# Kernel tuning notes

Hardware: AMD Instinct MI355X
Metric: run time of the kernel (lower is better)

Reference implementation:

```python
import jax, jax.numpy as jnp
import numpy as np

D_EMB = 1024
N_HEAD = 16
D_K = D_EMB // N_HEAD


def setup_inputs() -> dict:
    key = jax.random.key(0)
    ks = jax.random.split(key, 11)
    B, S = 2, 2048
    s = 1.0 / np.sqrt(D_EMB)
    inp = {
        'Q': jax.random.normal(ks[0], (B, S, D_EMB), jnp.float32),
        'K': jax.random.normal(ks[1], (B, S, D_EMB), jnp.float32),
        'V': jax.random.normal(ks[2], (B, S, D_EMB), jnp.float32),
        'W_Q': jax.random.normal(ks[3], (D_EMB, D_EMB), jnp.float32) * s,
        'b_Q': jax.random.normal(ks[4], (D_EMB,), jnp.float32) * s,
        'W_K': jax.random.normal(ks[5], (D_EMB, D_EMB), jnp.float32) * s,
        'b_K': jax.random.normal(ks[6], (D_EMB,), jnp.float32) * s,
        'W_V': jax.random.normal(ks[7], (D_EMB, D_EMB), jnp.float32) * s,
        'b_V': jax.random.normal(ks[8], (D_EMB,), jnp.float32) * s,
        'W_O': jax.random.normal(ks[9], (D_EMB, D_EMB), jnp.float32) * s,
        'b_O': jax.random.normal(ks[10], (D_EMB,), jnp.float32) * s,
    }
    return inp


def _heads(x):
    # [B, S, D] -> [B, H, S, d_k]
    B, S, _ = x.shape
    return x.reshape(B, S, N_HEAD, D_K).transpose(0, 2, 1, 3)


def reference(Q, K, V, W_Q, b_Q, W_K, b_K, W_V, b_V, W_O, b_O):
    q = _heads(Q @ W_Q.T + b_Q)
    k = _heads(K @ W_K.T + b_K)
    v = _heads(V @ W_V.T + b_V)
    scale = 1.0 / jnp.sqrt(jnp.asarray(D_K, q.dtype))
    scores = jnp.einsum('bhqd,bhkd->bhqk', q, k) * scale  # [B,H,S,S]
    probs = jax.nn.softmax(scores, axis=-1)
    attn = jnp.einsum('bhqk,bhkd->bhqd', probs, v)
    B, H, S, d = attn.shape
    attn = attn.transpose(0, 2, 1, 3).reshape(B, S, H * d)
    return attn @ W_O.T + b_O
```

## Files before the change

kernel.cpp:

```cpp
#include <hip/hip_runtime.h>
#include <cstdint>
#include <cstddef>

#define S_LEN 2048
#define NH    16
#define DKH   64
#define DEMB  1024
#define MTOT  4096

typedef float f32x4 __attribute__((ext_vector_type(4)));
typedef __bf16 bf16x8 __attribute__((ext_vector_type(8)));
typedef _Float16 f16;
typedef f16 f16x2 __attribute__((ext_vector_type(2)));
typedef f16 f16x4 __attribute__((ext_vector_type(4)));
typedef f16 f16x8 __attribute__((ext_vector_type(8)));
typedef unsigned short u16;
typedef unsigned int u32;
typedef u16 u16x8 __attribute__((ext_vector_type(8)));
typedef u16 u16x4 __attribute__((ext_vector_type(4)));
typedef u32 u32x4 __attribute__((ext_vector_type(4)));

static __device__ __forceinline__ u16 f2bf(float f) {
  u32 u = __builtin_bit_cast(u32, f);
  u += 0x7fffu + ((u >> 16) & 1u);
  return (u16)(u >> 16);
}
static __device__ __forceinline__ float bf2f(u16 b) {
  return __builtin_bit_cast(float, ((u32)b) << 16);
}
static __device__ __forceinline__ bf16x8 ldfrag(const u16* p) {
  return __builtin_bit_cast(bf16x8, *(const u16x8*)p);
}
static __device__ __forceinline__ f16x8 ldfragh8(const u16* p) {
  return __builtin_bit_cast(f16x8, *(const u16x8*)p);
}
static __device__ __forceinline__ f32x4 mfma16(bf16x8 a, bf16x8 b, f32x4 c) {
  return __builtin_amdgcn_mfma_f32_16x16x32_bf16(a, b, c, 0, 0, 0);
}
static __device__ __forceinline__ f32x4 mfmah32(f16x8 a, f16x8 b, f32x4 c) {
  return __builtin_amdgcn_mfma_f32_16x16x32_f16(a, b, c, 0, 0, 0);
}
static __device__ __forceinline__ void gl2lds16(const void* g, void* l) {
  __builtin_amdgcn_global_load_lds((__attribute__((address_space(1))) void*)g,
                                   (__attribute__((address_space(3))) void*)l,
                                   16, 0, 0);
}
static __device__ __forceinline__ u32 pkh2(float a, float b) {
  return __builtin_bit_cast(u32, __builtin_amdgcn_cvt_pkrtz(a, b));
}
static __device__ __forceinline__ f16x4 pkh4(float a, float b, float c, float d) {
  f16x2 lo = __builtin_bit_cast(f16x2, __builtin_amdgcn_cvt_pkrtz(a, b));
  f16x2 hi = __builtin_bit_cast(f16x2, __builtin_amdgcn_cvt_pkrtz(c, d));
  return __builtin_shufflevector(lo, hi, 0, 1, 2, 3);
}

#define SCL_Q (0.125f * 1.44269504088896340736f)

__global__ __launch_bounds__(256) void cvt_w(
    const float* __restrict__ wq, const float* __restrict__ wk,
    const float* __restrict__ wv, u16* __restrict__ dW) {
  const int b = blockIdx.x;
  const int seg = b >> 10;
  const float* s = (seg == 0) ? wq : (seg == 1) ? wk : wv;
  u16* d = dW + (size_t)seg * (DEMB * DEMB);
  const int i = ((b & 1023) * 256 + threadIdx.x) * 4;
  f32x4 f = *(const f32x4*)(s + i);
  u16x4 o;
  o[0] = f2bf(f[0]); o[1] = f2bf(f[1]); o[2] = f2bf(f[2]); o[3] = f2bf(f[3]);
  *(u16x4*)(d + i) = o;
}

__global__ __launch_bounds__(256) void qkv_gemm(
    const float* __restrict__ qf, const float* __restrict__ kf,
    const float* __restrict__ vf, const u16* __restrict__ W,
    const float* __restrict__ bq, const float* __restrict__ bk,
    const float* __restrict__ bv,
    u16* __restrict__ qh, u16* __restrict__ kh, u16* __restrict__ vt) {
  __shared__ __align__(16) u16 sA0[128 * 32], sA1[128 * 32];
  __shared__ __align__(16) u16 sB0[128 * 32], sB1[128 * 32];
  const int t = threadIdx.x;
  const int l = t & 63, w = t >> 6;
  const int ll = l & 15, lg = l >> 4;
  const int orig = blockIdx.x + 24 * blockIdx.y;
  const int xcd = orig & 7, q = orig >> 3;
  const int nb = q >> 2;
  const int mb = xcd * 4 + (q & 3);
  const int which = nb >> 3;
  const float* A = (which == 0) ? qf : ((which == 1) ? kf : vf);
  const int wr = (w >> 1) * 64, wc = (w & 1) * 64;

  f32x4 acc[4][4] = {};

  const int c0 = t, c1 = 256 + t;
  const int row0 = c0 >> 2, row1 = c1 >> 2;
  const int gc0 = (c0 & 3) ^ ((row0 >> 1) & 3);
  const int gc1 = (c1 & 3) ^ ((row1 >> 1) & 3);
  const float* asrc0 = A + (size_t)(mb * 128 + row0) * DEMB + gc0 * 8;
  const float* asrc1 = A + (size_t)(mb * 128 + row1) * DEMB + gc1 * 8;
  const u16* bsrc0 = W + (size_t)(nb * 128 + row0) * DEMB + gc0 * 8;
  const u16* bsrc1 = W + (size_t)(nb * 128 + row1) * DEMB + gc1 * 8;

  f32x4 va[4];
  auto LOADA = [&](int kt) {
    const int k0 = kt * 32;
    va[0] = *(const f32x4*)(asrc0 + k0);
    va[1] = *(const f32x4*)(asrc0 + k0 + 4);
    va[2] = *(const f32x4*)(asrc1 + k0);
    va[3] = *(const f32x4*)(asrc1 + k0 + 4);
  };
  auto STOREA = [&](u16* dA) {
#pragma unroll
    for (int i = 0; i < 2; ++i) {
      u16x8 o;
#pragma unroll
      for (int r = 0; r < 4; ++r) o[r] = f2bf(va[2 * i][r]);
#pragma unroll
      for (int r = 0; r < 4; ++r) o[4 + r] = f2bf(va[2 * i + 1][r]);
      *(u16x8*)&dA[(i * 256 + t) * 8] = o;
    }
  };
  auto STGB = [&](int kt, u16* dB) {
    const int k0 = kt * 32;
    gl2lds16(bsrc0 + k0, dB + c0 * 8);
    gl2lds16(bsrc1 + k0, dB + c1 * 8);
  };

  auto comp = [&](const u16* cA, const u16* cB) {
    bf16x8 af[4], bfr[4];
#pragma unroll
    for (int i2 = 0; i2 < 4; ++i2) {
      const int row = wr + i2 * 16 + ll;
      af[i2] = ldfrag(&cA[row * 32 + (lg ^ ((row >> 1) & 3)) * 8]);
    }
#pragma unroll
    for (int j2 = 0; j2 < 4; ++j2) {
      const int row = wc + j2 * 16 + ll;
      bfr[j2] = ldfrag(&cB[row * 32 + (lg ^ ((row >> 1) & 3)) * 8]);
    }
#pragma unroll
    for (int i2 = 0; i2 < 4; ++i2)
#pragma unroll
      for (int j2 = 0; j2 < 4; ++j2)
        acc[i2][j2] = mfma16(af[i2], bfr[j2], acc[i2][j2]);
  };

  LOADA(0); STGB(0, sB0); STOREA(sA0);
  __syncthreads();
  for (int kt2 = 0; kt2 < 16; ++kt2) {
    LOADA(2 * kt2 + 1);
    STGB(2 * kt2 + 1, sB1);
    comp(sA0, sB0);
    STOREA(sA1);
    __syncthreads();
    if (kt2 < 15) { LOADA(2 * kt2 + 2); STGB(2 * kt2 + 2, sB0); }
    comp(sA1, sB1);
    if (kt2 < 15) STOREA(sA0);
    __syncthreads();
  }

  const float* bias = (which == 0) ? bq : ((which == 1) ? bk : bv);
  const int b = (mb * 128) >> 11;

  if (which == 2) {
#pragma unroll
    for (int j2 = 0; j2 < 4; ++j2) {
      const int nl = (nb * 128 + wc + j2 * 16 + ll) & 1023;
      const int h = nl >> 6, dk = nl & 63;
      const float bb = bias[nl];
      u16* base = vt + ((size_t)((b * NH + h) * DKH + dk)) * S_LEN;
#pragma unroll
      for (int i2 = 0; i2 < 4; ++i2) {
        const int s = (mb * 128 + wr + i2 * 16 + lg * 4) & 2047;
        const f16x4 pk = pkh4(acc[i2][j2][0] + bb, acc[i2][j2][1] + bb,
                              acc[i2][j2][2] + bb, acc[i2][j2][3] + bb);
        *(u16x4*)&base[s] = __builtin_bit_cast(u16x4, pk);
      }
    }
  } else {
    u16* outp = (which == 0) ? qh : kh;
    const float scl = (which == 0) ? SCL_Q : 1.0f;
#pragma unroll
    for (int j2 = 0; j2 < 4; ++j2) {
      const int nl = (nb * 128 + wc + j2 * 16 + ll) & 1023;
      const int h = nl >> 6, dk = nl & 63;
      const float bb = bias[nl];
#pragma unroll
      for (int i2 = 0; i2 < 4; ++i2) {
#pragma unroll
        for (int r = 0; r < 4; ++r) {
          const int s = (mb * 128 + wr + i2 * 16 + lg * 4 + r) & 2047;
          const float val = (acc[i2][j2][r] + bb) * scl;
          outp[((size_t)((b * NH + h) * S_LEN + s)) * DKH + dk] = f2bf(val);
        }
      }
    }
  }
}

__global__ __launch_bounds__(512, 4) void attn_kernel(
    const u16* __restrict__ qh, const u16* __restrict__ kh,
    const u16* __restrict__ vt, u16* __restrict__ opart,
    float* __restrict__ lpart) {
  __shared__ __align__(16) u16 sK0[64 * 64], sK1[64 * 64];
  __shared__ __align__(16) u16 sV0[64 * 64], sV1[64 * 64];
  const int t = threadIdx.x;
  const int l = t & 63, w = t >> 6;
  const int ll = l & 15, lg = l >> 4;
  const int qb = blockIdx.x >> 1;
  const int ks = blockIdx.x & 1;
  const int q_blk = qb * 256;
  const int bh = blockIdx.y;

  bf16x8 aq[2][2];
#pragma unroll
  for (int qt = 0; qt < 2; ++qt) {
    const u16* qbase =
        qh + ((size_t)bh * S_LEN + q_blk + w * 32 + qt * 16 + ll) * DKH;
    aq[qt][0] = ldfrag(qbase + lg * 8);
    aq[qt][1] = ldfrag(qbase + 32 + lg * 8);
  }

  f32x4 oT[2][4] = {};
  float l_part[2] = {0.f, 0.f};

  const int strow = t >> 3;
  const int sgc = (t & 7) ^ (strow & 7);
  const u16* kstg =
      kh + ((size_t)bh * S_LEN + ks * 1024 + strow) * DKH + sgc * 8;
  const u16* vstg =
      vt + ((size_t)bh * DKH + strow) * S_LEN + ks * 1024 + sgc * 8;

  auto stg = [&](int kt, u16* dK, u16* dV) {
    gl2lds16(kstg + (size_t)kt * 64 * DKH, dK + t * 8);
    gl2lds16(vstg + kt * 64, dV + t * 8);
  };

  auto compute = [&](const u16* cK, const u16* cV) {
#pragma unroll
    for (int pr = 0; pr < 2; ++pr) {
      u32 pw0[4], pw1[4];
#pragma unroll
      for (int h = 0; h < 2; ++h) {
        const int krow = (pr * 2 + h) * 16 + ll;
        const bf16x8 ak0 = ldfrag(&cK[krow * 64 + (lg ^ (ll & 7)) * 8]);
        const bf16x8 ak1 = ldfrag(&cK[krow * 64 + ((4 + lg) ^ (ll & 7)) * 8]);
        f32x4 s0 = {}, s1 = {};
        s0 = mfma16(ak0, aq[0][0], s0);
        s0 = mfma16(ak1, aq[0][1], s0);
        s1 = mfma16(ak0, aq[1][0], s1);
        s1 = mfma16(ak1, aq[1][1], s1);
        {
          const float p0 = __builtin_amdgcn_exp2f(s0[0]);
          const float p1 = __builtin_amdgcn_exp2f(s0[1]);
          const float p2 = __builtin_amdgcn_exp2f(s0[2]);
          const float p3 = __builtin_amdgcn_exp2f(s0[3]);
          l_part[0] += (p0 + p1) + (p2 + p3);
          if (h == 0) { pw0[0] = pkh2(p0, p1); pw0[1] = pkh2(p2, p3); }
          else        { pw0[2] = pkh2(p0, p1); pw0[3] = pkh2(p2, p3); }
        }
        {
          const float p0 = __builtin_amdgcn_exp2f(s1[0]);
          const float p1 = __builtin_amdgcn_exp2f(s1[1]);
          const float p2 = __builtin_amdgcn_exp2f(s1[2]);
          const float p3 = __builtin_amdgcn_exp2f(s1[3]);
          l_part[1] += (p0 + p1) + (p2 + p3);
          if (h == 0) { pw1[0] = pkh2(p0, p1); pw1[1] = pkh2(p2, p3); }
          else        { pw1[2] = pkh2(p0, p1); pw1[3] = pkh2(p2, p3); }
        }
      }
      asm volatile("v_permlane32_swap_b32 %0, %1" : "+v"(pw0[0]), "+v"(pw0[2]));
      asm volatile("v_permlane16_swap_b32 %0, %1" : "+v"(pw0[0]), "+v"(pw0[2]));
      asm volatile("v_permlane32_swap_b32 %0, %1" : "+v"(pw0[1]), "+v"(pw0[3]));
      asm volatile("v_permlane16_swap_b32 %0, %1" : "+v"(pw0[1]), "+v"(pw0[3]));
      asm volatile("v_permlane32_swap_b32 %0, %1" : "+v"(pw1[0]), "+v"(pw1[2]));
      asm volatile("v_permlane16_swap_b32 %0, %1" : "+v"(pw1[0]), "+v"(pw1[2]));
      asm volatile("v_permlane32_swap_b32 %0, %1" : "+v"(pw1[1]), "+v"(pw1[3]));
      asm volatile("v_permlane16_swap_b32 %0, %1" : "+v"(pw1[1]), "+v"(pw1[3]));
      const f16x8 bp0 =
          __builtin_bit_cast(f16x8, (u32x4){pw0[0], pw0[1], pw0[2], pw0[3]});
      const f16x8 bp1 =
          __builtin_bit_cast(f16x8, (u32x4){pw1[0], pw1[1], pw1[2], pw1[3]});

#pragma unroll
      for (int nt = 0; nt < 4; ++nt) {
        const int row = nt * 16 + ll;
        const f16x8 av =
            ldfragh8(&cV[row * 64 + ((pr * 4 + lg) ^ (ll & 7)) * 8]);
        oT[0][nt] = mfmah32(av, bp0, oT[0][nt]);
        oT[1][nt] = mfmah32(av, bp1, oT[1][nt]);
      }
    }
  };

  stg(0, sK0, sV0);
  __syncthreads();
  for (int kt2 = 0; kt2 < 8; ++kt2) {
    stg(2 * kt2 + 1, sK1, sV1);
    compute(sK0, sV0);
    __syncthreads();
    if (kt2 < 7) stg(2 * kt2 + 2, sK0, sV0);
    compute(sK1, sV1);
    __syncthreads();
  }

#pragma unroll
  for (int qt = 0; qt < 2; ++qt) {
    float lv = l_part[qt];
    lv += __shfl_xor(lv, 16, 64);
    lv += __shfl_xor(lv, 32, 64);
    const int orow = q_blk + w * 32 + qt * 16 + ll;
    u16* obase = opart + (((size_t)(ks * 32 + bh)) * S_LEN + orow) * DKH;
#pragma unroll
    for (int nt = 0; nt < 4; ++nt) {
      u16x4 o;
#pragma unroll
      for (int r = 0; r < 4; ++r) o[r] = f2bf(oT[qt][nt][r]);
      *(u16x4*)&obase[nt * 16 + lg * 4] = o;
    }
    if (lg == 0) lpart[(ks * 32 + bh) * S_LEN + orow] = lv;
  }
}

__global__ __launch_bounds__(256) void merge_ctx(
    const u16* __restrict__ op, const float* __restrict__ lp,
    u16* __restrict__ ctx, const float* __restrict__ wo,
    u16* __restrict__ woBf) {
  if (blockIdx.x >= 2048) {
    const int i = ((blockIdx.x - 2048) * 256 + threadIdx.x) * 4;
    f32x4 f = *(const f32x4*)(wo + i);
    u16x4 o;
    o[0] = f2bf(f[0]); o[1] = f2bf(f[1]); o[2] = f2bf(f[2]); o[3] = f2bf(f[3]);
    *(u16x4*)(woBf + i) = o;
    return;
  }
  const int idx = blockIdx.x * 256 + threadIdx.x;
  const int dk8 = idx & 7;
  const int q = (idx >> 3) & 2047;
  const int bh = idx >> 14;
  const float inv = 1.0f / (lp[bh * S_LEN + q] + lp[(32 + bh) * S_LEN + q]);
  const u16x8 a = *(const u16x8*)&op[((size_t)bh * S_LEN + q) * DKH + dk8 * 8];
  const u16x8 c = *(const u16x8*)&op[((size_t)(32 + bh) * S_LEN + q) * DKH + dk8 * 8];
  u16x8 o;
#pragma unroll
  for (int r = 0; r < 8; ++r) o[r] = f2bf((bf2f(a[r]) + bf2f(c[r])) * inv);
  const int b = bh >> 4, h = bh & 15;
  *(u16x8*)&ctx[((size_t)((b * S_LEN + q) * NH + h)) * DKH + dk8 * 8] = o;
}

__global__ __launch_bounds__(256) void out_gemm(
    const u16* __restrict__ Am, const u16* __restrict__ W,
    const float* __restrict__ bo, float* __restrict__ out) {
  __shared__ __align__(16) u16 sA0[128 * 64], sA1[128 * 64];
  __shared__ __align__(16) u16 sB0[64 * 64], sB1[64 * 64];
  const int t = threadIdx.x;
  const int l = t & 63, w = t >> 6;
  const int ll = l & 15, lg = l >> 4;
  const int nb = blockIdx.x;
  const int mb = blockIdx.y;
  const int wr = (w >> 1) * 64, wc = (w & 1) * 32;

  f32x4 acc[4][2] = {};

  auto stg = [&](int kt, u16* dA, u16* dB) {
    const int k0 = kt * 64;
#pragma unroll
    for (int i = 0; i < 4; ++i) {
      const int c = i * 256 + t;
      const int row = c >> 3;
      const int gc = (c & 7) ^ (row & 7);
      gl2lds16(Am + (size_t)(mb * 128 + row) * DEMB + k0 + gc * 8, dA + c * 8);
      if (i < 2)
        gl2lds16(W + (size_t)(nb * 64 + row) * DEMB + k0 + gc * 8, dB + c * 8);
    }
  };

  auto comp = [&](const u16* cA, const u16* cB) {
#pragma unroll
    for (int kk = 0; kk < 2; ++kk) {
      bf16x8 af[4], bfr[2];
#pragma unroll
      for (int i2 = 0; i2 < 4; ++i2) {
        const int row = wr + i2 * 16 + ll;
        af[i2] = ldfrag(&cA[row * 64 + ((kk * 4 + lg) ^ (row & 7)) * 8]);
      }
#pragma unroll
      for (int j2 = 0; j2 < 2; ++j2) {
        const int row = wc + j2 * 16 + ll;
        bfr[j2] = ldfrag(&cB[row * 64 + ((kk * 4 + lg) ^ (row & 7)) * 8]);
      }
#pragma unroll
      for (int i2 = 0; i2 < 4; ++i2)
#pragma unroll
        for (int j2 = 0; j2 < 2; ++j2)
          acc[i2][j2] = mfma16(af[i2], bfr[j2], acc[i2][j2]);
    }
  };

  stg(0, sA0, sB0);
  __syncthreads();
  for (int kt2 = 0; kt2 < 8; ++kt2) {
    stg(2 * kt2 + 1, sA1, sB1);
    comp(sA0, sB0);
    __syncthreads();
    if (kt2 < 7) stg(2 * kt2 + 2, sA0, sB0);
    comp(sA1, sB1);
    __syncthreads();
  }

#pragma unroll
  for (int j2 = 0; j2 < 2; ++j2) {
    const int ncol = nb * 64 + wc + j2 * 16 + ll;
    const float bb = bo[ncol];
#pragma unroll
    for (int i2 = 0; i2 < 4; ++i2) {
#pragma unroll
      for (int r = 0; r < 4; ++r) {
        const int mrow = mb * 128 + wr + i2 * 16 + lg * 4 + r;
        out[(size_t)mrow * DEMB + ncol] = acc[i2][j2][r] + bb;
      }
    }
  }
}

extern "C" void kernel_launch(void* const* d_in, const int* in_sizes, int n_in,
                              void* d_out, int out_size, void* d_ws,
                              size_t ws_size, hipStream_t stream) {
  (void)in_sizes; (void)n_in; (void)out_size; (void)ws_size;
  const float* Q  = (const float*)d_in[0];
  const float* K  = (const float*)d_in[1];
  const float* V  = (const float*)d_in[2];
  const float* WQ = (const float*)d_in[3];
  const float* bQ = (const float*)d_in[4];
  const float* WK = (const float*)d_in[5];
  const float* bK = (const float*)d_in[6];
  const float* WV = (const float*)d_in[7];
  const float* bV = (const float*)d_in[8];
  const float* WO = (const float*)d_in[9];
  const float* bO = (const float*)d_in[10];
  float* out = (float*)d_out;

  u16* ws   = (u16*)d_ws;
  u16* Wqkv = ws;
  u16* WoBf = Wqkv + (size_t)3072 * 1024;
  u16* qh   = WoBf + (size_t)1024 * 1024;
  u16* kh   = qh + (size_t)32 * 2048 * 64;
  u16* vt   = kh + (size_t)32 * 2048 * 64;
  u16* ctx  = vt + (size_t)32 * 2048 * 64;
  u16* opart   = ctx + (size_t)MTOT * DEMB;
  float* lpart = (float*)(opart + (size_t)2 * 32 * 2048 * 64);

  cvt_w<<<3072, 256, 0, stream>>>(WQ, WK, WV, Wqkv);
  qkv_gemm<<<dim3(24, 32), 256, 0, stream>>>(Q, K, V, Wqkv, bQ, bK, bV,
                                             qh, kh, vt);
  attn_kernel<<<dim3(16, 32), 512, 0, stream>>>(qh, kh, vt, opart, lpart);
  merge_ctx<<<3072, 256, 0, stream>>>(opart, lpart, ctx, WO, WoBf);
  out_gemm<<<dim3(16, 32), 256, 0, stream>>>(ctx, WoBf, bO, out);
}
```

Baseline: 247.6 us.

## Stage fp32 activations via direct global-to-LDS loads in QKV GEMM; move Wo conversion

The QKV GEMM no longer loads fp32 activations into registers and converts them to bf16 before storing to LDS. It stages the raw fp32 tiles into LDS with direct global-to-LDS loads, using an XOR swizzle, and converts to bf16 while reading the MFMA fragments. This removes the register round trip and lets the A-tile loads run asynchronously like the B-tile loads. The cost is twice the LDS footprint and LDS read traffic for A, plus conversion work repeated across the warps that share rows. Separately, the Wo fp32-to-bf16 conversion moves from merge_ctx into the cvt_w kernel.

```diff
diff --git a/kernel.cpp b/kernel.cpp
--- a/kernel.cpp
+++ b/kernel.cpp
@@ -58,10 +58,11 @@
 
 __global__ __launch_bounds__(256) void cvt_w(
     const float* __restrict__ wq, const float* __restrict__ wk,
-    const float* __restrict__ wv, u16* __restrict__ dW) {
+    const float* __restrict__ wv, const float* __restrict__ wo,
+    u16* __restrict__ dW) {
   const int b = blockIdx.x;
   const int seg = b >> 10;
-  const float* s = (seg == 0) ? wq : (seg == 1) ? wk : wv;
+  const float* s = (seg == 0) ? wq : (seg == 1) ? wk : (seg == 2) ? wv : wo;
   u16* d = dW + (size_t)seg * (DEMB * DEMB);
   const int i = ((b & 1023) * 256 + threadIdx.x) * 4;
   f32x4 f = *(const f32x4*)(s + i);
@@ -76,7 +77,7 @@
     const float* __restrict__ bq, const float* __restrict__ bk,
     const float* __restrict__ bv,
     u16* __restrict__ qh, u16* __restrict__ kh, u16* __restrict__ vt) {
-  __shared__ __align__(16) u16 sA0[128 * 32], sA1[128 * 32];
+  __shared__ __align__(16) float sA0[128 * 32], sA1[128 * 32];
   __shared__ __align__(16) u16 sB0[128 * 32], sB1[128 * 32];
   const int t = threadIdx.x;
   const int l = t & 63, w = t >> 6;
@@ -91,46 +92,40 @@
 
   f32x4 acc[4][4] = {};
 
-  const int c0 = t, c1 = 256 + t;
-  const int row0 = c0 >> 2, row1 = c1 >> 2;
-  const int gc0 = (c0 & 3) ^ ((row0 >> 1) & 3);
-  const int gc1 = (c1 & 3) ^ ((row1 >> 1) & 3);
-  const float* asrc0 = A + (size_t)(mb * 128 + row0) * DEMB + gc0 * 8;
-  const float* asrc1 = A + (size_t)(mb * 128 + row1) * DEMB + gc1 * 8;
-  const u16* bsrc0 = W + (size_t)(nb * 128 + row0) * DEMB + gc0 * 8;
-  const u16* bsrc1 = W + (size_t)(nb * 128 + row1) * DEMB + gc1 * 8;
-
-  f32x4 va[4];
-  auto LOADA = [&](int kt) {
+  auto stgA = [&](int kt, float* dA) {
     const int k0 = kt * 32;
-    va[0] = *(const f32x4*)(asrc0 + k0);
-    va[1] = *(const f32x4*)(asrc0 + k0 + 4);
-    va[2] = *(const f32x4*)(asrc1 + k0);
-    va[3] = *(const f32x4*)(asrc1 + k0 + 4);
-  };
-  auto STOREA = [&](u16* dA) {
+#pragma unroll
+    for (int i = 0; i < 4; ++i) {
+      const int c = i * 256 + t;
+      const int row = c >> 3;
+      const int gc = (c & 7) ^ (row & 7);
+      gl2lds16(A + (size_t)(mb * 128 + row) * DEMB + k0 + gc * 4, &dA[c * 4]);
+    }
+  };
+  auto stgB = [&](int kt, u16* dB) {
+    const int k0 = kt * 32;
 #pragma unroll
     for (int i = 0; i < 2; ++i) {
-      u16x8 o;
-#pragma unroll
-      for (int r = 0; r < 4; ++r) o[r] = f2bf(va[2 * i][r]);
-#pragma unroll
-      for (int r = 0; r < 4; ++r) o[4 + r] = f2bf(va[2 * i + 1][r]);
-      *(u16x8*)&dA[(i * 256 + t) * 8] = o;
-    }
-  };
-  auto STGB = [&](int kt, u16* dB) {
-    const int k0 = kt * 32;
-    gl2lds16(bsrc0 + k0, dB + c0 * 8);
-    gl2lds16(bsrc1 + k0, dB + c1 * 8);
-  };
-
-  auto comp = [&](const u16* cA, const u16* cB) {
+      const int c = i * 256 + t;
+      const int row = c >> 2;
+      const int gc = (c & 3) ^ ((row >> 1) & 3);
+      gl2lds16(W + (size_t)(nb * 128 + row) * DEMB + k0 + gc * 8, dB + c * 8);
+    }
+  };
+
+  auto comp = [&](const float* cA, const u16* cB) {
     bf16x8 af[4], bfr[4];
 #pragma unroll
     for (int i2 = 0; i2 < 4; ++i2) {
       const int row = wr + i2 * 16 + ll;
-      af[i2] = ldfrag(&cA[row * 32 + (lg ^ ((row >> 1) & 3)) * 8]);
+      const f32x4 x0 = *(const f32x4*)&cA[row * 32 + ((2 * lg) ^ (row & 7)) * 4];
+      const f32x4 x1 = *(const f32x4*)&cA[row * 32 + ((2 * lg + 1) ^ (row & 7)) * 4];
+      u16x8 o;
+      o[0] = f2bf(x0[0]); o[1] = f2bf(x0[1]);
+      o[2] = f2bf(x0[2]); o[3] = f2bf(x0[3]);
+      o[4] = f2bf(x1[0]); o[5] = f2bf(x1[1]);
+      o[6] = f2bf(x1[2]); o[7] = f2bf(x1[3]);
+      af[i2] = __builtin_bit_cast(bf16x8, o);
     }
 #pragma unroll
     for (int j2 = 0; j2 < 4; ++j2) {
@@ -144,17 +139,14 @@
         acc[i2][j2] = mfma16(af[i2], bfr[j2], acc[i2][j2]);
   };
 
-  LOADA(0); STGB(0, sB0); STOREA(sA0);
+  stgA(0, sA0); stgB(0, sB0);
   __syncthreads();
   for (int kt2 = 0; kt2 < 16; ++kt2) {
-    LOADA(2 * kt2 + 1);
-    STGB(2 * kt2 + 1, sB1);
+    stgA(2 * kt2 + 1, sA1); stgB(2 * kt2 + 1, sB1);
     comp(sA0, sB0);
-    STOREA(sA1);
-    __syncthreads();
-    if (kt2 < 15) { LOADA(2 * kt2 + 2); STGB(2 * kt2 + 2, sB0); }
+    __syncthreads();
+    if (kt2 < 15) { stgA(2 * kt2 + 2, sA0); stgB(2 * kt2 + 2, sB0); }
     comp(sA1, sB1);
-    if (kt2 < 15) STOREA(sA0);
     __syncthreads();
   }
 
@@ -323,16 +315,7 @@
 
 __global__ __launch_bounds__(256) void merge_ctx(
     const u16* __restrict__ op, const float* __restrict__ lp,
-    u16* __restrict__ ctx, const float* __restrict__ wo,
-    u16* __restrict__ woBf) {
-  if (blockIdx.x >= 2048) {
-    const int i = ((blockIdx.x - 2048) * 256 + threadIdx.x) * 4;
-    f32x4 f = *(const f32x4*)(wo + i);
-    u16x4 o;
-    o[0] = f2bf(f[0]); o[1] = f2bf(f[1]); o[2] = f2bf(f[2]); o[3] = f2bf(f[3]);
-    *(u16x4*)(woBf + i) = o;
-    return;
-  }
+    u16* __restrict__ ctx) {
   const int idx = blockIdx.x * 256 + threadIdx.x;
   const int dk8 = idx & 7;
   const int q = (idx >> 3) & 2047;
@@ -441,18 +424,18 @@
 
   u16* ws   = (u16*)d_ws;
   u16* Wqkv = ws;
-  u16* WoBf = Wqkv + (size_t)3072 * 1024;
-  u16* qh   = WoBf + (size_t)1024 * 1024;
+  u16* Wo   = Wqkv + (size_t)3072 * 1024;
+  u16* qh   = Wo + (size_t)1024 * 1024;
   u16* kh   = qh + (size_t)32 * 2048 * 64;
   u16* vt   = kh + (size_t)32 * 2048 * 64;
   u16* ctx  = vt + (size_t)32 * 2048 * 64;
   u16* opart   = ctx + (size_t)MTOT * DEMB;
   float* lpart = (float*)(opart + (size_t)2 * 32 * 2048 * 64);
 
-  cvt_w<<<3072, 256, 0, stream>>>(WQ, WK, WV, Wqkv);
+  cvt_w<<<4096, 256, 0, stream>>>(WQ, WK, WV, WO, Wqkv);
   qkv_gemm<<<dim3(24, 32), 256, 0, stream>>>(Q, K, V, Wqkv, bQ, bK, bV,
                                              qh, kh, vt);
   attn_kernel<<<dim3(16, 32), 512, 0, stream>>>(qh, kh, vt, opart, lpart);
-  merge_ctx<<<3072, 256, 0, stream>>>(opart, lpart, ctx, WO, WoBf);
-  out_gemm<<<dim3(16, 32), 256, 0, stream>>>(ctx, WoBf, bO, out);
-}
+  merge_ctx<<<2048, 256, 0, stream>>>(opart, lpart, ctx);
+  out_gemm<<<dim3(16, 32), 256, 0, stream>>>(ctx, Wo, bO, out);
+}
```

Result: faster. 222.8 us, median of 2 (-10.0%).
